# Kernel optimization log

Measured on AMD Instinct MI355X. Metric: run time of the kernel, lower is better.

Reference implementation:

```python
import jax, jax.numpy as jnp
import numpy as np

# loss hyperparams (from init_kwargs / KeypointsMSESmoothLoss defaults in source)
SCALE_KPS = 0.1
THRESHOLD = 100.0
ALPHA = 0.1
BETA = 0.9

B, V, J = 8192, 8, 32


def setup_inputs() -> dict:
    key = jax.random.key(0)
    k1, k2, k3, k4 = jax.random.split(key, 4)
    # realistic pinhole intrinsics, broadcast per batch/view
    f, cx, cy = 1500.0, 500.0, 500.0
    K_base = jnp.array([[f, 0.0, cx], [0.0, f, cy], [0.0, 0.0, 1.0]], jnp.float32)
    K = jnp.broadcast_to(K_base, (B, V, 3, 3)) + 0.01 * jax.random.normal(k1, (B, V, 3, 3), jnp.float32)
    # camera extrinsics [R|t]; push t_z positive so points sit in front of camera
    cam_preds = 0.1 * jax.random.normal(k2, (B, V, 3, 4), jnp.float32)
    cam_preds = cam_preds.at[..., 2, 3].add(10.0)
    kps_world_pred = jax.random.normal(k3, (B, J, 3), jnp.float32)
    initial_keypoints = 100.0 * jax.random.normal(k4, (B, V, J, 2), jnp.float32)
    return {"K": K, "cam_preds": cam_preds, "kps_world_pred": kps_world_pred,
            "initial_keypoints": initial_keypoints}


def reference(K, cam_preds, kps_world_pred, initial_keypoints):
    b, v = cam_preds.shape[0], cam_preds.shape[1]
    # project_to_weak_views: world -> camera -> image, perspective divide
    ones = jnp.ones_like(kps_world_pred[..., :1])
    Xh = jnp.concatenate([kps_world_pred, ones], axis=-1)          # [B,J,4]
    cam_pts = jnp.einsum('bvij,bnj->bvni', cam_preds, Xh)          # [B,V,J,3]
    img_pts = jnp.einsum('bvij,bvnj->bvni', K, cam_pts)            # [B,V,J,3]
    proj = img_pts[..., :2] / img_pts[..., 2:3]                    # [B,V,J,2]
    # penalization: |fro_norm(proj)/fro_norm(init) - 1| per (batch, view)
    pn = jnp.linalg.norm(proj.reshape(b, v, -1), axis=-1)
    inorm = jnp.linalg.norm(initial_keypoints.reshape(b, v, -1), axis=-1)
    penal = jnp.abs(pn / inorm - 1.0)                              # [B,V]
    # KeypointsMSESmoothLoss on scaled keypoints (no validity mask)
    diff = ((proj - initial_keypoints) * SCALE_KPS) ** 2           # [B,V,J,2]
    over = diff > THRESHOLD
    safe = jnp.where(over, diff, THRESHOLD)
    diff = jnp.where(over, safe ** ALPHA * THRESHOLD ** BETA, diff)
    per_view_loss = diff.sum(axis=(-1, -2)) / 2.0                  # dimension = last dim = 2
    return jnp.mean(per_view_loss * penal)
```

## Files before the change

### kernel.cpp

```cpp
#include <hip/hip_runtime.h>
#include <math.h>

#define B_TOT 8192
#define V_N 8
#define J_N 32

#define SCALE_KPS 0.1f
#define THRESH 100.0f
#define THRESH_BETA 63.09573444801932f

__device__ __forceinline__ float smooth_term(float d) {
    return (d > THRESH)
        ? __builtin_amdgcn_exp2f(0.1f * __builtin_amdgcn_logf(d)) * THRESH_BETA
        : d;
}

__global__ __launch_bounds__(256) void qpl_fused(
    const float* __restrict__ Kmat,
    const float* __restrict__ cam,
    const float* __restrict__ kps,
    const float* __restrict__ init,
    float* __restrict__ partial)
{
    __shared__ float s_acc[4];

    const int tid  = threadIdx.x;
    const int wave = tid >> 6;
    const int lane = tid & 63;
    const int jj   = lane & 31;
    const int h    = lane >> 5;
    const int b    = blockIdx.x * 4 + wave;

    const float* kp = kps + b * (J_N * 3) + jj * 3;
    const float x = kp[0];
    const float y = kp[1];
    const float z = kp[2];

    const float*  camb  = cam  + (size_t)b * (V_N * 12);
    const float*  Kb    = Kmat + (size_t)b * (V_N * 9);
    const float2* initb = (const float2*)(init + (size_t)b * (V_N * J_N * 2));

    float acc = 0.0f;

    #pragma unroll
    for (int vi = 0; vi < 4; ++vi) {
        const int v = h + vi * 2;

        const float4 c0 = ((const float4*)(camb + v * 12))[0];
        const float4 c1 = ((const float4*)(camb + v * 12))[1];
        const float4 c2 = ((const float4*)(camb + v * 12))[2];
        const float* kv = Kb + v * 9;
        const float k0 = kv[0], k1 = kv[1], k2 = kv[2];
        const float k3 = kv[3], k4 = kv[4], k5 = kv[5];
        const float k6 = kv[6], k7 = kv[7], k8 = kv[8];

        const float2 ik = initb[v * J_N + jj];

        const float cp0 = c0.x * x + c0.y * y + c0.z * z + c0.w;
        const float cp1 = c1.x * x + c1.y * y + c1.z * z + c1.w;
        const float cp2 = c2.x * x + c2.y * y + c2.z * z + c2.w;

        const float i0 = k0 * cp0 + k1 * cp1 + k2 * cp2;
        const float i1 = k3 * cp0 + k4 * cp1 + k5 * cp2;
        const float i2 = k6 * cp0 + k7 * cp1 + k8 * cp2;

        float r = __builtin_amdgcn_rcpf(i2);
        r = r * (2.0f - i2 * r);
        const float p0 = i0 * r;
        const float p1 = i1 * r;

        float d0 = (p0 - ik.x) * SCALE_KPS; d0 *= d0;
        float d1 = (p1 - ik.y) * SCALE_KPS; d1 *= d1;

        float sum_diff = smooth_term(d0) + smooth_term(d1);
        float sum_p2   = p0 * p0 + p1 * p1;
        float sum_i2   = ik.x * ik.x + ik.y * ik.y;

        #pragma unroll
        for (int m = 16; m >= 1; m >>= 1) {
            sum_diff += __shfl_xor(sum_diff, m);
            sum_p2   += __shfl_xor(sum_p2, m);
            sum_i2   += __shfl_xor(sum_i2, m);
        }
        const float penal = fabsf(sqrtf(sum_p2 / sum_i2) - 1.0f);
        acc += (sum_diff * 0.5f) * penal;
    }

    acc += __shfl_xor(acc, 32);

    if (lane == 0) s_acc[wave] = acc;
    __syncthreads();
    if (tid == 0)
        partial[blockIdx.x] = s_acc[0] + s_acc[1] + s_acc[2] + s_acc[3];
}

__global__ __launch_bounds__(256) void qpl_reduce(
    const float* __restrict__ partial, float* __restrict__ out)
{
    __shared__ float s_w[4];
    float t = 0.0f;
    #pragma unroll
    for (int k = 0; k < 8; ++k) t += partial[threadIdx.x + k * 256];

    #pragma unroll
    for (int m = 32; m >= 1; m >>= 1) t += __shfl_xor(t, m);

    if ((threadIdx.x & 63) == 0) s_w[threadIdx.x >> 6] = t;
    __syncthreads();

    if (threadIdx.x == 0) {
        const float tot = s_w[0] + s_w[1] + s_w[2] + s_w[3];
        out[0] = tot * (1.0f / (float)(B_TOT * V_N));
    }
}

extern "C" void kernel_launch(void* const* d_in, const int* in_sizes, int n_in,
                              void* d_out, int out_size, void* d_ws, size_t ws_size,
                              hipStream_t stream) {
    const float* Kmat = (const float*)d_in[0];
    const float* cam  = (const float*)d_in[1];
    const float* kps  = (const float*)d_in[2];
    const float* init = (const float*)d_in[3];
    float* partial = (float*)d_ws;
    float* out     = (float*)d_out;

    qpl_fused<<<B_TOT / 4, 256, 0, stream>>>(Kmat, cam, kps, init, partial);
    qpl_reduce<<<1, 256, 0, stream>>>(partial, out);
}
```

Measured before the change: 79.85 us.

## Remap lanes to one view per 8-lane group with vectorized loads

Each wavefront now gives 8 lanes to each view, and each lane handles 4 joints. Keypoints and initial keypoints are loaded as float4 instead of scattered scalar/float2 loads. Camera and intrinsics are loaded once per lane instead of per view iteration, and the per-view shuffle reduction shrinks from 5 steps times 4 views to 3 steps. It also drops the Newton refinement of the reciprocal and uses a fast rcp for the norm ratio, which slightly lowers numerical precision.

```diff
diff --git a/kernel.cpp b/kernel.cpp
--- a/kernel.cpp
+++ b/kernel.cpp
@@ -27,65 +27,68 @@
     const int tid  = threadIdx.x;
     const int wave = tid >> 6;
     const int lane = tid & 63;
-    const int jj   = lane & 31;
-    const int h    = lane >> 5;
+    const int v    = lane >> 3;
+    const int t    = lane & 7;
     const int b    = blockIdx.x * 4 + wave;
 
-    const float* kp = kps + b * (J_N * 3) + jj * 3;
-    const float x = kp[0];
-    const float y = kp[1];
-    const float z = kp[2];
+    const float4* kp4 = (const float4*)(kps + (size_t)b * (J_N * 3) + t * 12);
+    const float4 f0 = kp4[0], f1 = kp4[1], f2 = kp4[2];
 
-    const float*  camb  = cam  + (size_t)b * (V_N * 12);
-    const float*  Kb    = Kmat + (size_t)b * (V_N * 9);
-    const float2* initb = (const float2*)(init + (size_t)b * (V_N * J_N * 2));
+    const float* cv = cam + (size_t)b * (V_N * 12) + v * 12;
+    const float4 c0 = ((const float4*)cv)[0];
+    const float4 c1 = ((const float4*)cv)[1];
+    const float4 c2 = ((const float4*)cv)[2];
 
-    float acc = 0.0f;
+    const float* kv = Kmat + (size_t)b * (V_N * 9) + v * 9;
+    const float k0 = kv[0], k1 = kv[1], k2 = kv[2];
+    const float k3 = kv[3], k4 = kv[4], k5 = kv[5];
+    const float k6 = kv[6], k7 = kv[7], k8 = kv[8];
+
+    const float4* ib = (const float4*)(init + (size_t)b * (V_N * J_N * 2) + lane * 8);
+    const float4 q0 = ib[0], q1 = ib[1];
+
+    const float xs[4]  = {f0.x, f0.w, f1.z, f2.y};
+    const float ys[4]  = {f0.y, f1.x, f1.w, f2.z};
+    const float zs[4]  = {f0.z, f1.y, f2.x, f2.w};
+    const float ikx[4] = {q0.x, q0.z, q1.x, q1.z};
+    const float iky[4] = {q0.y, q0.w, q1.y, q1.w};
+
+    float sum_diff = 0.0f, sum_p2 = 0.0f, sum_i2 = 0.0f;
 
     #pragma unroll
-    for (int vi = 0; vi < 4; ++vi) {
-        const int v = h + vi * 2;
-
-        const float4 c0 = ((const float4*)(camb + v * 12))[0];
-        const float4 c1 = ((const float4*)(camb + v * 12))[1];
-        const float4 c2 = ((const float4*)(camb + v * 12))[2];
-        const float* kv = Kb + v * 9;
-        const float k0 = kv[0], k1 = kv[1], k2 = kv[2];
-        const float k3 = kv[3], k4 = kv[4], k5 = kv[5];
-        const float k6 = kv[6], k7 = kv[7], k8 = kv[8];
-
-        const float2 ik = initb[v * J_N + jj];
-
-        const float cp0 = c0.x * x + c0.y * y + c0.z * z + c0.w;
-        const float cp1 = c1.x * x + c1.y * y + c1.z * z + c1.w;
-        const float cp2 = c2.x * x + c2.y * y + c2.z * z + c2.w;
+    for (int m = 0; m < 4; ++m) {
+        const float cp0 = c0.x * xs[m] + c0.y * ys[m] + c0.z * zs[m] + c0.w;
+        const float cp1 = c1.x * xs[m] + c1.y * ys[m] + c1.z * zs[m] + c1.w;
+        const float cp2 = c2.x * xs[m] + c2.y * ys[m] + c2.z * zs[m] + c2.w;
 
         const float i0 = k0 * cp0 + k1 * cp1 + k2 * cp2;
         const float i1 = k3 * cp0 + k4 * cp1 + k5 * cp2;
         const float i2 = k6 * cp0 + k7 * cp1 + k8 * cp2;
 
-        float r = __builtin_amdgcn_rcpf(i2);
-        r = r * (2.0f - i2 * r);
+        const float r  = __builtin_amdgcn_rcpf(i2);
         const float p0 = i0 * r;
         const float p1 = i1 * r;
 
-        float d0 = (p0 - ik.x) * SCALE_KPS; d0 *= d0;
-        float d1 = (p1 - ik.y) * SCALE_KPS; d1 *= d1;
+        float d0 = (p0 - ikx[m]) * SCALE_KPS; d0 *= d0;
+        float d1 = (p1 - iky[m]) * SCALE_KPS; d1 *= d1;
 
-        float sum_diff = smooth_term(d0) + smooth_term(d1);
-        float sum_p2   = p0 * p0 + p1 * p1;
-        float sum_i2   = ik.x * ik.x + ik.y * ik.y;
-
-        #pragma unroll
-        for (int m = 16; m >= 1; m >>= 1) {
-            sum_diff += __shfl_xor(sum_diff, m);
-            sum_p2   += __shfl_xor(sum_p2, m);
-            sum_i2   += __shfl_xor(sum_i2, m);
-        }
-        const float penal = fabsf(sqrtf(sum_p2 / sum_i2) - 1.0f);
-        acc += (sum_diff * 0.5f) * penal;
+        sum_diff += smooth_term(d0) + smooth_term(d1);
+        sum_p2   += p0 * p0 + p1 * p1;
+        sum_i2   += ikx[m] * ikx[m] + iky[m] * iky[m];
     }
 
+    #pragma unroll
+    for (int m = 1; m <= 4; m <<= 1) {
+        sum_diff += __shfl_xor(sum_diff, m);
+        sum_p2   += __shfl_xor(sum_p2, m);
+        sum_i2   += __shfl_xor(sum_i2, m);
+    }
+
+    const float penal = fabsf(sqrtf(sum_p2 * __builtin_amdgcn_rcpf(sum_i2)) - 1.0f);
+    float acc = (sum_diff * 0.5f) * penal;
+
+    acc += __shfl_xor(acc, 8);
+    acc += __shfl_xor(acc, 16);
     acc += __shfl_xor(acc, 32);
 
     if (lane == 0) s_acc[wave] = acc;
```

New measurement: 77.35 us (median of 2 runs). 3.1% less time.
